# Optimization experiments

Hardware: AMD Instinct MI355X
Metric: run time of the kernel (lower is better)

The kernel has to match this reference:

```python
import jax, jax.numpy as jnp
import numpy as np

B, S, D = 2, 2048, 2048
H, KVH, HD = 32, 8, 64  # n_heads, n_kv_heads, head_dim
REP = H // KVH


def setup_inputs() -> dict:
    key = jax.random.key(0)
    k0, k1, k2, k3, k4 = jax.random.split(key, 5)
    x = jax.random.normal(k0, (B, S, D), dtype=jnp.float32)
    # Linear weights stored as (in, out); matches torch nn.Linear(in,out).weight.T
    scale = 1.0 / np.sqrt(D)
    wq = jax.random.normal(k1, (D, H * HD), dtype=jnp.float32) * scale
    wk = jax.random.normal(k2, (D, KVH * HD), dtype=jnp.float32) * scale
    wv = jax.random.normal(k3, (D, KVH * HD), dtype=jnp.float32) * scale
    wo = jax.random.normal(k4, (H * HD, D), dtype=jnp.float32) * scale
    mask = jnp.tril(jnp.ones((S, S), dtype=bool))[None, None]  # [1,1,S,S] causal
    return {"x": x, "wq": wq, "wk": wk, "wv": wv, "wo": wo, "mask": mask}


def reference(x, wq, wk, wv, wo, mask):
    # Projections
    q = (x @ wq).reshape(B, S, KVH, REP, HD)   # Q head h = g*REP + r -> group g
    k = (x @ wk).reshape(B, S, KVH, HD)
    v = (x @ wv).reshape(B, S, KVH, HD)
    # Grouped attention: never materialize repeated K/V (same math as repeat_kv)
    scores = jnp.einsum('bqgrd,bkgd->bgrqk', q, k) / jnp.sqrt(jnp.asarray(HD, x.dtype))
    m = mask[:, :, None]  # [1,1,1,S,S] broadcasts over (group, rep)
    scores = jnp.where(m, scores, -jnp.inf)
    probs = jax.nn.softmax(scores, axis=-1)  # [B,KVH,REP,S,S]
    out = jnp.einsum('bgrqk,bkgd->bqgrd', probs, v)  # [B,S,KVH,REP,HD]
    out = out.reshape(B, S, H * HD)
    return out @ wo
```

## Files before the change

kernel.cpp:

```cpp
#include <hip/hip_runtime.h>
#include <stdint.h>

typedef __bf16 bf16x8 __attribute__((ext_vector_type(8)));
typedef float  f32x4  __attribute__((ext_vector_type(4)));
typedef float  f32x16 __attribute__((ext_vector_type(16)));

#define QSCALE 0.18033688011112042f

typedef __attribute__((address_space(1))) const void* as1cv;
typedef __attribute__((address_space(3))) void*       as3v;

__device__ __forceinline__ void gload16(const void* g, void* l) {
  __builtin_amdgcn_global_load_lds((as1cv)g, (as3v)l, 16, 0, 0);
}

__device__ __forceinline__ unsigned short f2b(float f) {
  union { float f; unsigned int u; } v; v.f = f;
  unsigned int r = v.u + 0x7fffu + ((v.u >> 16) & 1u);
  return (unsigned short)(r >> 16);
}

__device__ __forceinline__ float b2f(unsigned short s) {
  union { unsigned int u; float f; } v; v.u = (unsigned int)s << 16;
  return v.f;
}

#if __has_builtin(__builtin_amdgcn_exp2f)
__device__ __forceinline__ float fexp2(float x) { return __builtin_amdgcn_exp2f(x); }
#else
__device__ __forceinline__ float fexp2(float x) {
  float r;
  asm volatile("v_exp_f32 %0, %1\n\ts_nop 1" : "=v"(r) : "v"(x));
  return r;
}
#endif

__global__ void detect_dtype(const unsigned short* __restrict__ x, int* __restrict__ flag) {
  const int t = threadIdx.x;
  bool big = false;
  for (int i = t; i < 1024; i += 64) {
    float f = b2f(x[i]);
    if (!(fabsf(f) < 1e6f)) big = true;
  }
  if (t == 0) *flag = 0;
  __syncthreads();
  if (__any(big) && t == 0) *flag = 1;
}

__global__ __launch_bounds__(256) void convert_x(const void* __restrict__ src,
                                                 unsigned short* __restrict__ dst,
                                                 const int* __restrict__ flag) {
  const int i = blockIdx.x * 256 + threadIdx.x;
  if (*flag) {
    float4 a = ((const float4*)src)[2 * i];
    float4 b = ((const float4*)src)[2 * i + 1];
    union { unsigned short o[8]; uint4 v; } u;
    u.o[0] = f2b(a.x); u.o[1] = f2b(a.y); u.o[2] = f2b(a.z); u.o[3] = f2b(a.w);
    u.o[4] = f2b(b.x); u.o[5] = f2b(b.y); u.o[6] = f2b(b.z); u.o[7] = f2b(b.w);
    ((uint4*)dst)[i] = u.v;
  } else {
    ((uint4*)dst)[i] = ((const uint4*)src)[i];
  }
}

__global__ __launch_bounds__(256) void transpose_w(const void* __restrict__ src, int R, int C,
                                                   unsigned short* __restrict__ dst,
                                                   const int* __restrict__ flag) {
  __shared__ unsigned short tile[64][72];
  const int t = threadIdx.x;
  const int r = t >> 2;
  const int c0 = (t & 3) << 4;
  const int gr = blockIdx.y * 64 + r;
  const int gc = blockIdx.x * 64 + c0;
  if (*flag) {
    const float* s = (const float*)src + (size_t)gr * C + gc;
#pragma unroll
    for (int j = 0; j < 16; j += 4) {
      float4 v = *(const float4*)(s + j);
      tile[r][c0 + j + 0] = f2b(v.x);
      tile[r][c0 + j + 1] = f2b(v.y);
      tile[r][c0 + j + 2] = f2b(v.z);
      tile[r][c0 + j + 3] = f2b(v.w);
    }
  } else {
    const unsigned short* s = (const unsigned short*)src + (size_t)gr * C + gc;
    *(uint4*)&tile[r][c0]     = *(const uint4*)s;
    *(uint4*)&tile[r][c0 + 8] = *(const uint4*)(s + 8);
  }
  __syncthreads();
  const int c    = t >> 2;
  const int rblk = (t & 3) << 4;
  union { unsigned short o[16]; uint4 v[2]; } u;
#pragma unroll
  for (int j = 0; j < 16; ++j) u.o[j] = tile[rblk + j][c];
  unsigned short* d = dst + (size_t)(blockIdx.x * 64 + c) * R + blockIdx.y * 64 + rblk;
  *(uint4*)d       = u.v[0];
  *(uint4*)(d + 8) = u.v[1];
}

__global__ __launch_bounds__(256) void gemm_bt2(const unsigned short* __restrict__ A,
                                                const unsigned short* __restrict__ Bt,
                                                void* __restrict__ Cv,
                                                unsigned short* __restrict__ vtout,
                                                int M, int N, int K, int scale_cols,
                                                const int* __restrict__ f32flag) {
  __shared__ unsigned short As[2][128 * 64];
  __shared__ unsigned short Bs[2][128 * 64];
  const int t = threadIdx.x;
  const int lane = t & 63;
  const int wave = t >> 6;
  const int wm = wave >> 1, wn = wave & 1;
  int bx, by;
  {
    const int nx = (int)gridDim.x;
    const int nwg = nx * (int)gridDim.y;
    const int wg = (int)blockIdx.y * nx + (int)blockIdx.x;
    const int cpx = nwg >> 3;
    const int swz = (wg & 7) * cpx + (wg >> 3);
    bx = swz % nx; by = swz / nx;
  }
  const int m0 = by * 128, n0 = bx * 128;
  const int fr = lane & 15;
  const int kb = (lane >> 4) << 4;

  int rowS[4], dofS[4], scS[4];
#pragma unroll
  for (int i = 0; i < 4; ++i) {
    int off = i * 4096 + t * 16;
    dofS[i] = off;
    rowS[i] = off >> 7;
    scS[i]  = (off & 127) ^ ((rowS[i] & 7) << 4);
  }
  const char* pA[4];
  const char* pB[4];
#pragma unroll
  for (int i = 0; i < 4; ++i) {
    pA[i] = (const char*)(A  + (size_t)(m0 + rowS[i]) * K) + scS[i];
    pB[i] = (const char*)(Bt + (size_t)(n0 + rowS[i]) * K) + scS[i];
  }

  f32x4 acc[4][4] = {};
  const int NT = K >> 6;

#pragma unroll
  for (int i = 0; i < 4; ++i) {
    gload16(pA[i], (char*)As[0] + dofS[i]);
    gload16(pB[i], (char*)Bs[0] + dofS[i]);
  }
  __syncthreads();

  for (int kt = 0; kt < NT; ++kt) {
    if (kt + 1 < NT) {
      const int kby = (kt + 1) * 128;
      const int bsel = (kt + 1) & 1;
#pragma unroll
      for (int i = 0; i < 4; ++i) {
        gload16(pA[i] + kby, (char*)As[bsel] + dofS[i]);
        gload16(pB[i] + kby, (char*)Bs[bsel] + dofS[i]);
      }
    }
    const char* Ab = (const char*)As[kt & 1];
    const char* Bb = (const char*)Bs[kt & 1];
#pragma unroll
    for (int ks = 0; ks < 2; ++ks) {
      bf16x8 af[4], bfv[4];
#pragma unroll
      for (int i = 0; i < 4; ++i) {
        const int ra = wm * 64 + i * 16 + fr;
        af[i] = *(const bf16x8*)(Ab + ra * 128 + ((ks * 64 + kb) ^ ((ra & 7) << 4)));
        const int rb = wn * 64 + i * 16 + fr;
        bfv[i] = *(const bf16x8*)(Bb + rb * 128 + ((ks * 64 + kb) ^ ((rb & 7) << 4)));
      }
      __builtin_amdgcn_s_setprio(1);
#pragma unroll
      for (int i = 0; i < 4; ++i)
#pragma unroll
        for (int j = 0; j < 4; ++j)
          acc[i][j] = __builtin_amdgcn_mfma_f32_16x16x32_bf16(af[i], bfv[j], acc[i][j], 0, 0, 0);
      __builtin_amdgcn_s_setprio(0);
    }
    __syncthreads();
  }

  const int cm0 = m0 + wm * 64 + ((lane >> 4) << 2);
  const int cn0 = n0 + wn * 64 + fr;
  if (vtout && n0 >= 2560) {
    const int bb = m0 >> 11;
#pragma unroll
    for (int i = 0; i < 4; ++i) {
      const int s0 = cm0 + i * 16;
#pragma unroll
      for (int j = 0; j < 4; ++j) {
        const int d = cn0 + j * 16 - 2560;
        uint2 pr;
        pr.x = (unsigned int)f2b(acc[i][j][0]) | ((unsigned int)f2b(acc[i][j][1]) << 16);
        pr.y = (unsigned int)f2b(acc[i][j][2]) | ((unsigned int)f2b(acc[i][j][3]) << 16);
        *(uint2*)(vtout + (size_t)(bb * 512 + d) * 2048 + (s0 & 2047)) = pr;
      }
    }
    return;
  }
  const bool of32 = f32flag && (*f32flag != 0);
  if (of32) {
    float* C = (float*)Cv;
#pragma unroll
    for (int i = 0; i < 4; ++i)
#pragma unroll
      for (int j = 0; j < 4; ++j) {
        float sc = (cn0 + j * 16 < scale_cols) ? QSCALE : 1.0f;
#pragma unroll
        for (int r = 0; r < 4; ++r)
          C[(size_t)(cm0 + i * 16 + r) * N + (cn0 + j * 16)] = acc[i][j][r] * sc;
      }
  } else {
    unsigned short* C = (unsigned short*)Cv;
#pragma unroll
    for (int i = 0; i < 4; ++i)
#pragma unroll
      for (int j = 0; j < 4; ++j) {
        float sc = (cn0 + j * 16 < scale_cols) ? QSCALE : 1.0f;
#pragma unroll
        for (int r = 0; r < 4; ++r)
          C[(size_t)(cm0 + i * 16 + r) * N + (cn0 + j * 16)] = f2b(acc[i][j][r] * sc);
      }
  }
}

__global__ __launch_bounds__(256, 4) void attn_fwd7(const unsigned short* __restrict__ qkv,
                                                    const unsigned short* __restrict__ vt,
                                                    unsigned short* __restrict__ ob) {
  __shared__ unsigned short Ks[2][64 * 64];
  __shared__ unsigned short Vs[2][64 * 64];
  const int t = threadIdx.x, lane = t & 63, w = t >> 6;
  const int half = lane >> 5, q32 = lane & 31;
  const int lin = (int)blockIdx.x;
  const int rr = lin >> 8;
  const int k  = (lin & 255) >> 4;
  const int gb = lin & 15;
  const int g = gb & 7, b = gb >> 3;
  const int qt = (rr == 0) ? 63 - k : (rr == 1) ? 32 + k : (rr == 2) ? 31 - k : k;
  const int h = g * 4 + w;
  const size_t bS = (size_t)b * 2048;
  const size_t vtb = ((size_t)((b << 3) + g)) * 64;
  const int nkt = (qt >> 1) + 1;
  const int q_glob = qt * 32 + q32;

  int rowS[2], dofS[2], cbS[2];
#pragma unroll
  for (int i = 0; i < 2; ++i) {
    int off = i * 4096 + t * 16;
    dofS[i] = off;
    rowS[i] = off >> 7;
    cbS[i]  = (off & 127) ^ ((rowS[i] & 7) << 4);
  }

  bf16x8 qf[4];
  {
    const unsigned short* qrow = qkv + (bS + q_glob) * 3072 + h * 64 + half * 8;
#pragma unroll
    for (int c = 0; c < 4; ++c) qf[c] = *(const bf16x8*)(qrow + 16 * c);
  }
  const unsigned short* kp[2];
  const unsigned short* vp[2];
#pragma unroll
  for (int i = 0; i < 2; ++i) {
    kp[i] = qkv + (bS + rowS[i]) * 3072 + 2048 + g * 64 + (cbS[i] >> 1);
    vp[i] = vt + (vtb + rowS[i]) * 2048 + (cbS[i] >> 1);
  }
  f32x16 Ot0 = {}, Ot1 = {};
  float m_run = -1e30f, l_run = 0.f;

#pragma unroll
  for (int i = 0; i < 2; ++i) {
    gload16(kp[i], (char*)Ks[0] + dofS[i]);
    gload16(vp[i], (char*)Vs[0] + dofS[i]);
    kp[i] += 64 * 3072;
    vp[i] += 64;
  }
  int cur = 0;
  for (int kt = 0; kt < nkt; ++kt) {
    __syncthreads();
    if (kt + 1 < nkt) {
#pragma unroll
      for (int i = 0; i < 2; ++i) {
        gload16(kp[i], (char*)Ks[cur ^ 1] + dofS[i]);
        gload16(vp[i], (char*)Vs[cur ^ 1] + dofS[i]);
        kp[i] += 64 * 3072;
        vp[i] += 64;
      }
    }
    const char* Kb = (const char*)Ks[cur];
    const char* Vb = (const char*)Vs[cur];
    const int sk0 = 2 * kt, sk1 = 2 * kt + 1;
    const bool do1 = (sk1 <= qt);

    f32x16 s0 = {}, s1 = {};
    {
      const int kr0 = q32;
      const int ksw0 = (kr0 & 7) << 4;
      bf16x8 ka0 = *(const bf16x8*)(Kb + kr0 * 128 + ((16 * half) ^ ksw0));
      bf16x8 ka1 = *(const bf16x8*)(Kb + kr0 * 128 + ((32 + 16 * half) ^ ksw0));
      bf16x8 ka2 = *(const bf16x8*)(Kb + kr0 * 128 + ((64 + 16 * half) ^ ksw0));
      bf16x8 ka3 = *(const bf16x8*)(Kb + kr0 * 128 + ((96 + 16 * half) ^ ksw0));
      __builtin_amdgcn_s_setprio(1);
      s0 = __builtin_amdgcn_mfma_f32_32x32x16_bf16(ka0, qf[0], s0, 0, 0, 0);
      s0 = __builtin_amdgcn_mfma_f32_32x32x16_bf16(ka1, qf[1], s0, 0, 0, 0);
      s0 = __builtin_amdgcn_mfma_f32_32x32x16_bf16(ka2, qf[2], s0, 0, 0, 0);
      s0 = __builtin_amdgcn_mfma_f32_32x32x16_bf16(ka3, qf[3], s0, 0, 0, 0);
      __builtin_amdgcn_s_setprio(0);
    }
    if (do1) {
      const int kr1 = 32 + q32;
      const int ksw1 = (kr1 & 7) << 4;
      bf16x8 kb0 = *(const bf16x8*)(Kb + kr1 * 128 + ((16 * half) ^ ksw1));
      bf16x8 kb1 = *(const bf16x8*)(Kb + kr1 * 128 + ((32 + 16 * half) ^ ksw1));
      bf16x8 kb2 = *(const bf16x8*)(Kb + kr1 * 128 + ((64 + 16 * half) ^ ksw1));
      bf16x8 kb3 = *(const bf16x8*)(Kb + kr1 * 128 + ((96 + 16 * half) ^ ksw1));
      __builtin_amdgcn_s_setprio(1);
      s1 = __builtin_amdgcn_mfma_f32_32x32x16_bf16(kb0, qf[0], s1, 0, 0, 0);
      s1 = __builtin_amdgcn_mfma_f32_32x32x16_bf16(kb1, qf[1], s1, 0, 0, 0);
      s1 = __builtin_amdgcn_mfma_f32_32x32x16_bf16(kb2, qf[2], s1, 0, 0, 0);
      s1 = __builtin_amdgcn_mfma_f32_32x32x16_bf16(kb3, qf[3], s1, 0, 0, 0);
      __builtin_amdgcn_s_setprio(0);
    }
    const int qrel = q32 - 4 * half;
    if (sk0 == qt) {
#pragma unroll
      for (int r = 0; r < 16; ++r) {
        const int pat = (r & 3) + 8 * (r >> 2);
        if (pat > qrel) s0[r] = -1e30f;
      }
    }
    if (do1 && sk1 == qt) {
#pragma unroll
      for (int r = 0; r < 16; ++r) {
        const int pat = (r & 3) + 8 * (r >> 2);
        if (pat > qrel) s1[r] = -1e30f;
      }
    }
    float tm[8];
#pragma unroll
    for (int r = 0; r < 8; ++r) tm[r] = fmaxf(s0[r], s0[r + 8]);
    if (do1) {
#pragma unroll
      for (int r = 0; r < 8; ++r) tm[r] = fmaxf(tm[r], fmaxf(s1[r], s1[r + 8]));
    }
#pragma unroll
    for (int r = 0; r < 4; ++r) tm[r] = fmaxf(tm[r], tm[r + 4]);
    float pm = fmaxf(fmaxf(tm[0], tm[1]), fmaxf(tm[2], tm[3]));
    pm = fmaxf(pm, __shfl_xor(pm, 32, 64));
    if (!__all(pm - m_run <= 8.f)) {
      const float mn = fmaxf(m_run, pm);
      const float corr = fexp2(m_run - mn);
      m_run = mn;
      l_run *= corr;
#pragma unroll
      for (int r = 0; r < 16; ++r) { Ot0[r] *= corr; Ot1[r] *= corr; }
    }
    float ts[8];
#pragma unroll
    for (int r = 0; r < 16; ++r) s0[r] = fexp2(s0[r] - m_run);
    if (do1) {
#pragma unroll
      for (int r = 0; r < 16; ++r) s1[r] = fexp2(s1[r] - m_run);
    }
#pragma unroll
    for (int r = 0; r < 8; ++r) ts[r] = s0[r] + s0[r + 8];
    if (do1) {
#pragma unroll
      for (int r = 0; r < 8; ++r) ts[r] += s1[r] + s1[r + 8];
    }
#pragma unroll
    for (int r = 0; r < 4; ++r) ts[r] += ts[r + 4];
    float rs = (ts[0] + ts[1]) + (ts[2] + ts[3]);
    rs += __shfl_xor(rs, 32, 64);
    l_run += rs;
    bf16x8 pf0, pf1, pf2, pf3;
    {
      unsigned int a01, a23, a45, a67;
      asm("v_cvt_pk_bf16_f32 %0, %1, %2" : "=v"(a01) : "v"(s0[0]), "v"(s0[1]));
      asm("v_cvt_pk_bf16_f32 %0, %1, %2" : "=v"(a23) : "v"(s0[2]), "v"(s0[3]));
      asm("v_cvt_pk_bf16_f32 %0, %1, %2" : "=v"(a45) : "v"(s0[4]), "v"(s0[5]));
      asm("v_cvt_pk_bf16_f32 %0, %1, %2" : "=v"(a67) : "v"(s0[6]), "v"(s0[7]));
      asm("v_permlane32_swap_b32 %0, %1" : "+v"(a01), "+v"(a45));
      asm("v_permlane32_swap_b32 %0, %1" : "+v"(a23), "+v"(a67));
      union { unsigned int u[4]; bf16x8 v; } fu;
      fu.u[0] = a01; fu.u[1] = a23; fu.u[2] = a45; fu.u[3] = a67;
      pf0 = fu.v;
      asm("v_cvt_pk_bf16_f32 %0, %1, %2" : "=v"(a01) : "v"(s0[8]),  "v"(s0[9]));
      asm("v_cvt_pk_bf16_f32 %0, %1, %2" : "=v"(a23) : "v"(s0[10]), "v"(s0[11]));
      asm("v_cvt_pk_bf16_f32 %0, %1, %2" : "=v"(a45) : "v"(s0[12]), "v"(s0[13]));
      asm("v_cvt_pk_bf16_f32 %0, %1, %2" : "=v"(a67) : "v"(s0[14]), "v"(s0[15]));
      asm("v_permlane32_swap_b32 %0, %1" : "+v"(a01), "+v"(a45));
      asm("v_permlane32_swap_b32 %0, %1" : "+v"(a23), "+v"(a67));
      fu.u[0] = a01; fu.u[1] = a23; fu.u[2] = a45; fu.u[3] = a67;
      pf1 = fu.v;
    }
    if (do1) {
      unsigned int a01, a23, a45, a67;
      asm("v_cvt_pk_bf16_f32 %0, %1, %2" : "=v"(a01) : "v"(s1[0]), "v"(s1[1]));
      asm("v_cvt_pk_bf16_f32 %0, %1, %2" : "=v"(a23) : "v"(s1[2]), "v"(s1[3]));
      asm("v_cvt_pk_bf16_f32 %0, %1, %2" : "=v"(a45) : "v"(s1[4]), "v"(s1[5]));
      asm("v_cvt_pk_bf16_f32 %0, %1, %2" : "=v"(a67) : "v"(s1[6]), "v"(s1[7]));
      asm("v_permlane32_swap_b32 %0, %1" : "+v"(a01), "+v"(a45));
      asm("v_permlane32_swap_b32 %0, %1" : "+v"(a23), "+v"(a67));
      union { unsigned int u[4]; bf16x8 v; } fu;
      fu.u[0] = a01; fu.u[1] = a23; fu.u[2] = a45; fu.u[3] = a67;
      pf2 = fu.v;
      asm("v_cvt_pk_bf16_f32 %0, %1, %2" : "=v"(a01) : "v"(s1[8]),  "v"(s1[9]));
      asm("v_cvt_pk_bf16_f32 %0, %1, %2" : "=v"(a23) : "v"(s1[10]), "v"(s1[11]));
      asm("v_cvt_pk_bf16_f32 %0, %1, %2" : "=v"(a45) : "v"(s1[12]), "v"(s1[13]));
      asm("v_cvt_pk_bf16_f32 %0, %1, %2" : "=v"(a67) : "v"(s1[14]), "v"(s1[15]));
      asm("v_permlane32_swap_b32 %0, %1" : "+v"(a01), "+v"(a45));
      asm("v_permlane32_swap_b32 %0, %1" : "+v"(a23), "+v"(a67));
      fu.u[0] = a01; fu.u[1] = a23; fu.u[2] = a45; fu.u[3] = a67;
      pf3 = fu.v;
    }
    const int vsw0 = (q32 & 7) << 4;
    {
      const int cbase = 16 * half;
      bf16x8 vf00 = *(const bf16x8*)(Vb + q32 * 128 + (cbase ^ vsw0));
      bf16x8 vf01 = *(const bf16x8*)(Vb + q32 * 128 + ((cbase + 32) ^ vsw0));
      bf16x8 vf10 = *(const bf16x8*)(Vb + (32 + q32) * 128 + (cbase ^ vsw0));
      bf16x8 vf11 = *(const bf16x8*)(Vb + (32 + q32) * 128 + ((cbase + 32) ^ vsw0));
      __builtin_amdgcn_s_setprio(1);
      Ot0 = __builtin_amdgcn_mfma_f32_32x32x16_bf16(vf00, pf0, Ot0, 0, 0, 0);
      Ot0 = __builtin_amdgcn_mfma_f32_32x32x16_bf16(vf01, pf1, Ot0, 0, 0, 0);
      Ot1 = __builtin_amdgcn_mfma_f32_32x32x16_bf16(vf10, pf0, Ot1, 0, 0, 0);
      Ot1 = __builtin_amdgcn_mfma_f32_32x32x16_bf16(vf11, pf1, Ot1, 0, 0, 0);
      __builtin_amdgcn_s_setprio(0);
    }
    if (do1) {
      const int cbase = 64 + 16 * half;
      bf16x8 vf00 = *(const bf16x8*)(Vb + q32 * 128 + (cbase ^ vsw0));
      bf16x8 vf01 = *(const bf16x8*)(Vb + q32 * 128 + ((cbase + 32) ^ vsw0));
      bf16x8 vf10 = *(const bf16x8*)(Vb + (32 + q32) * 128 + (cbase ^ vsw0));
      bf16x8 vf11 = *(const bf16x8*)(Vb + (32 + q32) * 128 + ((cbase + 32) ^ vsw0));
      __builtin_amdgcn_s_setprio(1);
      Ot0 = __builtin_amdgcn_mfma_f32_32x32x16_bf16(vf00, pf2, Ot0, 0, 0, 0);
      Ot0 = __builtin_amdgcn_mfma_f32_32x32x16_bf16(vf01, pf3, Ot0, 0, 0, 0);
      Ot1 = __builtin_amdgcn_mfma_f32_32x32x16_bf16(vf10, pf2, Ot1, 0, 0, 0);
      Ot1 = __builtin_amdgcn_mfma_f32_32x32x16_bf16(vf11, pf3, Ot1, 0, 0, 0);
      __builtin_amdgcn_s_setprio(0);
    }
    cur ^= 1;
  }
  const float inv = 1.f / l_run;
  unsigned short* orow = ob + (bS + q_glob) * 2048 + h * 64;
#pragma unroll
  for (int j = 0; j < 4; ++j) {
    uint2 pr;
    pr.x = (unsigned int)f2b(Ot0[4 * j + 0] * inv) | ((unsigned int)f2b(Ot0[4 * j + 1] * inv) << 16);
    pr.y = (unsigned int)f2b(Ot0[4 * j + 2] * inv) | ((unsigned int)f2b(Ot0[4 * j + 3] * inv) << 16);
    *(uint2*)(orow + 8 * j + 4 * half) = pr;
    uint2 pr2;
    pr2.x = (unsigned int)f2b(Ot1[4 * j + 0] * inv) | ((unsigned int)f2b(Ot1[4 * j + 1] * inv) << 16);
    pr2.y = (unsigned int)f2b(Ot1[4 * j + 2] * inv) | ((unsigned int)f2b(Ot1[4 * j + 3] * inv) << 16);
    *(uint2*)(orow + 32 + 8 * j + 4 * half) = pr2;
  }
}

extern "C" void kernel_launch(void* const* d_in, const int* in_sizes, int n_in,
                              void* d_out, int out_size, void* d_ws, size_t ws_size,
                              hipStream_t stream) {
  (void)in_sizes; (void)n_in; (void)out_size; (void)ws_size;
  const void* x  = d_in[0];
  const void* wq = d_in[1];
  const void* wk = d_in[2];
  const void* wv = d_in[3];
  const void* wo = d_in[4];
  unsigned short* ws = (unsigned short*)d_ws;

  int* FLAG = (int*)ws;
  unsigned short* WT  = ws + 128;
  unsigned short* WOT = WT  + (size_t)3072 * 2048;
  unsigned short* QKV = WOT + (size_t)2048 * 2048;
  unsigned short* VT  = QKV + (size_t)4096 * 3072;
  unsigned short* OB  = VT  + (size_t)16 * 64 * 2048;
  unsigned short* XB  = OB;

  detect_dtype<<<1, 64, 0, stream>>>((const unsigned short*)x, FLAG);

  transpose_w<<<dim3(32, 32), 256, 0, stream>>>(wq, 2048, 2048, WT, FLAG);
  transpose_w<<<dim3(8, 32), 256, 0, stream>>>(wk, 2048, 512, WT + (size_t)2048 * 2048, FLAG);
  transpose_w<<<dim3(8, 32), 256, 0, stream>>>(wv, 2048, 512, WT + (size_t)2560 * 2048, FLAG);
  transpose_w<<<dim3(32, 32), 256, 0, stream>>>(wo, 2048, 2048, WOT, FLAG);
  convert_x<<<4096, 256, 0, stream>>>(x, XB, FLAG);

  gemm_bt2<<<dim3(24, 32), 256, 0, stream>>>(XB, WT, QKV, VT, 4096, 3072, 2048, 2048, nullptr);
  attn_fwd7<<<dim3(1024), 256, 0, stream>>>(QKV, VT, OB);
  gemm_bt2<<<dim3(16, 32), 256, 0, stream>>>(OB, WOT, d_out, nullptr, 4096, 2048, 2048, 0, FLAG);
}
```

Measured before the change: 181.0 us.

## Add 256x256-tile 8-wave QKV GEMM and merge weight transposes into one launch

Replaces the 128x128-tile QKV projection GEMM with a new 512-thread kernel using 256x256 tiles, 16x16x32 MFMAs and explicit vmcnt-based double buffering. The aim is more data reuse per LDS load and fewer workgroups. The four weight transpose launches are merged into a single 3D-grid launch, and blocks past the narrower matrices exit early. The larger tile means only 192 workgroups, which may underfill the GPU's CUs, and it needs 128KB of LDS per block.

```diff
diff --git a/kernel.cpp b/kernel.cpp
--- a/kernel.cpp
+++ b/kernel.cpp
@@ -63,9 +63,24 @@
   }
 }
 
-__global__ __launch_bounds__(256) void transpose_w(const void* __restrict__ src, int R, int C,
-                                                   unsigned short* __restrict__ dst,
-                                                   const int* __restrict__ flag) {
+__global__ __launch_bounds__(256) void transpose_w4(const void* __restrict__ wq,
+                                                    const void* __restrict__ wk,
+                                                    const void* __restrict__ wv,
+                                                    const void* __restrict__ wo,
+                                                    unsigned short* __restrict__ WT,
+                                                    unsigned short* __restrict__ WOT,
+                                                    const int* __restrict__ flag) {
+  const int z = blockIdx.z;
+  const void* src;
+  unsigned short* dst;
+  int C;
+  const int R = 2048;
+  if (z == 0)      { src = wq; dst = WT;                            C = 2048; }
+  else if (z == 1) { src = wk; dst = WT + (size_t)2048 * 2048;      C = 512;  }
+  else if (z == 2) { src = wv; dst = WT + (size_t)2560 * 2048;      C = 512;  }
+  else             { src = wo; dst = WOT;                           C = 2048; }
+  if ((int)blockIdx.x * 64 >= C) return;
+
   __shared__ unsigned short tile[64][72];
   const int t = threadIdx.x;
   const int r = t >> 2;
@@ -96,6 +111,142 @@
   unsigned short* d = dst + (size_t)(blockIdx.x * 64 + c) * R + blockIdx.y * 64 + rblk;
   *(uint4*)d       = u.v[0];
   *(uint4*)(d + 8) = u.v[1];
+}
+
+__global__ __launch_bounds__(512, 2) void gemm_qkv8(const unsigned short* __restrict__ A,
+                                                    const unsigned short* __restrict__ Bt,
+                                                    void* __restrict__ Cv,
+                                                    unsigned short* __restrict__ vtout,
+                                                    int M, int N, int K, int scale_cols,
+                                                    const int* __restrict__ f32flag) {
+  __shared__ unsigned short As[2][256 * 64];
+  __shared__ unsigned short Bs[2][256 * 64];
+  const int t = threadIdx.x;
+  const int lane = t & 63;
+  const int wave = t >> 6;
+  const int wm = wave >> 2, wn = wave & 3;
+  int bx, by;
+  {
+    const int nx = (int)gridDim.x;
+    const int nwg = nx * (int)gridDim.y;
+    const int wg = (int)blockIdx.y * nx + (int)blockIdx.x;
+    const int cpx = nwg >> 3;
+    const int swz = (wg & 7) * cpx + (wg >> 3);
+    bx = swz % nx; by = swz / nx;
+  }
+  const int m0 = by * 256, n0 = bx * 256;
+  const int fr = lane & 15;
+  const int kb = (lane >> 4) << 4;
+
+  int rowS[4], dofS[4], scS[4];
+#pragma unroll
+  for (int i = 0; i < 4; ++i) {
+    int off = i * 8192 + t * 16;
+    dofS[i] = off;
+    rowS[i] = off >> 7;
+    scS[i]  = (off & 127) ^ ((rowS[i] & 7) << 4);
+  }
+  const char* pA[4];
+  const char* pB[4];
+#pragma unroll
+  for (int i = 0; i < 4; ++i) {
+    pA[i] = (const char*)(A  + (size_t)(m0 + rowS[i]) * K) + scS[i];
+    pB[i] = (const char*)(Bt + (size_t)(n0 + rowS[i]) * K) + scS[i];
+  }
+
+  f32x4 acc[8][4] = {};
+  const int NT = K >> 6;
+
+#pragma unroll
+  for (int i = 0; i < 4; ++i) {
+    gload16(pA[i], (char*)As[0] + dofS[i]);
+    gload16(pB[i], (char*)Bs[0] + dofS[i]);
+  }
+
+  for (int kt = 0; kt < NT; ++kt) {
+    if (kt + 1 < NT) {
+      const int kby = (kt + 1) * 128;
+      const int bsel = (kt + 1) & 1;
+#pragma unroll
+      for (int i = 0; i < 4; ++i) {
+        gload16(pA[i] + kby, (char*)As[bsel] + dofS[i]);
+        gload16(pB[i] + kby, (char*)Bs[bsel] + dofS[i]);
+      }
+      asm volatile("s_waitcnt vmcnt(8)" ::: "memory");
+    } else {
+      asm volatile("s_waitcnt vmcnt(0)" ::: "memory");
+    }
+    __builtin_amdgcn_s_barrier();
+    __builtin_amdgcn_sched_barrier(0);
+    const char* Ab = (const char*)As[kt & 1];
+    const char* Bb = (const char*)Bs[kt & 1];
+#pragma unroll
+    for (int ks = 0; ks < 2; ++ks) {
+      bf16x8 af[8], bfv[4];
+#pragma unroll
+      for (int i = 0; i < 8; ++i) {
+        const int ra = wm * 128 + i * 16 + fr;
+        af[i] = *(const bf16x8*)(Ab + ra * 128 + ((ks * 64 + kb) ^ ((ra & 7) << 4)));
+      }
+#pragma unroll
+      for (int j = 0; j < 4; ++j) {
+        const int rb = wn * 64 + j * 16 + fr;
+        bfv[j] = *(const bf16x8*)(Bb + rb * 128 + ((ks * 64 + kb) ^ ((rb & 7) << 4)));
+      }
+      __builtin_amdgcn_s_setprio(1);
+#pragma unroll
+      for (int i = 0; i < 8; ++i)
+#pragma unroll
+        for (int j = 0; j < 4; ++j)
+          acc[i][j] = __builtin_amdgcn_mfma_f32_16x16x32_bf16(af[i], bfv[j], acc[i][j], 0, 0, 0);
+      __builtin_amdgcn_s_setprio(0);
+    }
+    __builtin_amdgcn_s_barrier();
+    __builtin_amdgcn_sched_barrier(0);
+  }
+
+  const int cm0 = m0 + wm * 128 + ((lane >> 4) << 2);
+  const int cn0 = n0 + wn * 64 + fr;
+  if (vtout && n0 >= 2560) {
+    const int bb = m0 >> 11;
+#pragma unroll
+    for (int i = 0; i < 8; ++i) {
+      const int s0 = cm0 + i * 16;
+#pragma unroll
+      for (int j = 0; j < 4; ++j) {
+        const int d = cn0 + j * 16 - 2560;
+        uint2 pr;
+        pr.x = (unsigned int)f2b(acc[i][j][0]) | ((unsigned int)f2b(acc[i][j][1]) << 16);
+        pr.y = (unsigned int)f2b(acc[i][j][2]) | ((unsigned int)f2b(acc[i][j][3]) << 16);
+        *(uint2*)(vtout + (size_t)(bb * 512 + d) * 2048 + (s0 & 2047)) = pr;
+      }
+    }
+    return;
+  }
+  const bool of32 = f32flag && (*f32flag != 0);
+  if (of32) {
+    float* C = (float*)Cv;
+#pragma unroll
+    for (int i = 0; i < 8; ++i)
+#pragma unroll
+      for (int j = 0; j < 4; ++j) {
+        float sc = (cn0 + j * 16 < scale_cols) ? QSCALE : 1.0f;
+#pragma unroll
+        for (int r = 0; r < 4; ++r)
+          C[(size_t)(cm0 + i * 16 + r) * N + (cn0 + j * 16)] = acc[i][j][r] * sc;
+      }
+  } else {
+    unsigned short* C = (unsigned short*)Cv;
+#pragma unroll
+    for (int i = 0; i < 8; ++i)
+#pragma unroll
+      for (int j = 0; j < 4; ++j) {
+        float sc = (cn0 + j * 16 < scale_cols) ? QSCALE : 1.0f;
+#pragma unroll
+        for (int r = 0; r < 4; ++r)
+          C[(size_t)(cm0 + i * 16 + r) * N + (cn0 + j * 16)] = f2b(acc[i][j][r] * sc);
+      }
+  }
 }
 
 __global__ __launch_bounds__(256) void gemm_bt2(const unsigned short* __restrict__ A,
@@ -291,7 +442,7 @@
     }
     const char* Kb = (const char*)Ks[cur];
     const char* Vb = (const char*)Vs[cur];
-    const int sk0 = 2 * kt, sk1 = 2 * kt + 1;
+    const int sk1 = 2 * kt + 1;
     const bool do1 = (sk1 <= qt);
 
     f32x16 s0 = {}, s1 = {};
@@ -324,7 +475,7 @@
       __builtin_amdgcn_s_setprio(0);
     }
     const int qrel = q32 - 4 * half;
-    if (sk0 == qt) {
+    if (2 * kt == qt) {
 #pragma unroll
       for (int r = 0; r < 16; ++r) {
         const int pat = (r & 3) + 8 * (r >> 2);
@@ -480,14 +631,10 @@
   unsigned short* XB  = OB;
 
   detect_dtype<<<1, 64, 0, stream>>>((const unsigned short*)x, FLAG);
-
-  transpose_w<<<dim3(32, 32), 256, 0, stream>>>(wq, 2048, 2048, WT, FLAG);
-  transpose_w<<<dim3(8, 32), 256, 0, stream>>>(wk, 2048, 512, WT + (size_t)2048 * 2048, FLAG);
-  transpose_w<<<dim3(8, 32), 256, 0, stream>>>(wv, 2048, 512, WT + (size_t)2560 * 2048, FLAG);
-  transpose_w<<<dim3(32, 32), 256, 0, stream>>>(wo, 2048, 2048, WOT, FLAG);
+  transpose_w4<<<dim3(32, 32, 4), 256, 0, stream>>>(wq, wk, wv, wo, WT, WOT, FLAG);
   convert_x<<<4096, 256, 0, stream>>>(x, XB, FLAG);
 
-  gemm_bt2<<<dim3(24, 32), 256, 0, stream>>>(XB, WT, QKV, VT, 4096, 3072, 2048, 2048, nullptr);
+  gemm_qkv8<<<dim3(12, 16), 512, 0, stream>>>(XB, WT, QKV, VT, 4096, 3072, 2048, 2048, nullptr);
   attn_fwd7<<<dim3(1024), 256, 0, stream>>>(QKV, VT, OB);
   gemm_bt2<<<dim3(16, 32), 256, 0, stream>>>(OB, WOT, d_out, nullptr, 4096, 2048, 2048, 0, FLAG);
 }
```

Measured after the change: 186.4 us. +3.0%, slower.
